# Performance work log

Hardware: AMD Instinct MI355X
Metric: run time of the kernel (lower is better)

Reference implementation:

```python
import jax, jax.numpy as jnp
import numpy as np

SEQ, B, DIM, UNITS = 256, 64, 1024, 1024


def setup_inputs() -> dict:
    key = jax.random.key(0)
    k1, k2, k3, k4, k5, k6 = jax.random.split(key, 6)
    s = 1.0 / np.sqrt(UNITS)
    x = jax.random.normal(k1, (SEQ, B, DIM), dtype=jnp.float32)
    hx = jnp.zeros((B, UNITS), dtype=jnp.float32)
    cx = jnp.zeros((B, UNITS), dtype=jnp.float32)
    reset = (jax.random.uniform(k2, (SEQ, B, 1)) < 0.05).astype(jnp.float32)
    W_ih = jax.random.uniform(k3, (4 * UNITS, DIM), minval=-s, maxval=s, dtype=jnp.float32)
    W_hh = jax.random.uniform(k4, (4 * UNITS, UNITS), minval=-s, maxval=s, dtype=jnp.float32)
    b_ih = jax.random.uniform(k5, (4 * UNITS,), minval=-s, maxval=s, dtype=jnp.float32)
    b_hh = jax.random.uniform(k6, (4 * UNITS,), minval=-s, maxval=s, dtype=jnp.float32)
    return {"x": x, "hx": hx, "cx": cx, "reset": reset,
            "W_ih": W_ih, "W_hh": W_hh, "b_ih": b_ih, "b_hh": b_hh}


def _lstm_scan(x, hx, cx, mask, W_ih, W_hh, b_ih, b_hh):
    # Precompute input projections for all timesteps in one big GEMM:
    # [seq, b, dim] @ [dim, 4u] -> [seq, b, 4u]
    x_proj = jnp.einsum('sbd,gd->sbg', x, W_ih) + b_ih + b_hh

    def step(carry, inp):
        h, c = carry
        xp_t, m_t = inp               # xp_t: [b, 4u], m_t: [b, 1]
        h = h * m_t                   # reset hidden/cell state at episode starts
        c = c * m_t
        gates = xp_t + h @ W_hh.T     # [b, 4u]
        i, f, g, o = jnp.split(gates, 4, axis=-1)  # torch LSTMCell gate order
        i = jax.nn.sigmoid(i)
        f = jax.nn.sigmoid(f)
        g = jnp.tanh(g)
        o = jax.nn.sigmoid(o)
        c = f * c + i * g
        h = o * jnp.tanh(c)
        return (h, c), (h, c)

    (_, _), (hs, cs) = jax.lax.scan(step, (hx, cx), (x_proj, mask))
    return hs, cs  # each [seq, b, units]


def reference(x, hx, cx, reset, W_ih, W_hh, b_ih, b_hh):
    mask = 1.0 - reset  # [seq, b, 1]
    hs, cs = _lstm_scan(x, hx, cx, mask, W_ih, W_hh, b_ih, b_hh)
    # original returns (stacked outputs, per-step (h, c) states)
    return hs, hs, cs
```

## Files before the change

### kernel.cpp

```cpp
#include <hip/hip_runtime.h>
#include <stdint.h>

typedef unsigned short ushort_t;
typedef __attribute__((ext_vector_type(8))) short s16x8;
typedef __attribute__((ext_vector_type(4))) float f32x4;
typedef __attribute__((ext_vector_type(4))) unsigned short u16x4;

#define TO_GLB(p) ((const __attribute__((address_space(1))) void*)(p))
#define TO_LDS(p) ((__attribute__((address_space(3))) void*)(p))

__device__ __forceinline__ ushort_t f2bf(float f) {
  union { float f; uint32_t u; } v; v.f = f;
  uint32_t u = v.u;
  uint32_t r = (u + 0x7FFFu + ((u >> 16) & 1u)) >> 16;
  return (ushort_t)r;
}
__device__ __forceinline__ float bf2f(ushort_t b) {
  union { uint32_t u; float f; } v; v.u = ((uint32_t)b) << 16;
  return v.f;
}
__device__ __forceinline__ float sigm(float x) {
  x = fminf(fmaxf(x, -30.f), 30.f);
  return 1.0f / (1.0f + __expf(-x));
}
__device__ __forceinline__ float tanh_f(float x) {
  x = fminf(fmaxf(x, -15.f), 15.f);
  float t = __expf(2.0f * x);
  return (t - 1.0f) / (t + 1.0f);
}

__global__ void conv_f32_to_bf16(const float* __restrict__ src,
                                 ushort_t* __restrict__ dst, int n4) {
  int i = blockIdx.x * blockDim.x + threadIdx.x;
  if (i < n4) {
    float4 v = ((const float4*)src)[i];
    u16x4 o;
    o[0] = f2bf(v.x); o[1] = f2bf(v.y); o[2] = f2bf(v.z); o[3] = f2bf(v.w);
    *(u16x4*)(dst + 4 * (size_t)i) = o;
  }
}

__global__ void init_h(const float* __restrict__ hx, ushort_t* __restrict__ h0, int n) {
  int i = blockIdx.x * blockDim.x + threadIdx.x;
  if (i < n) h0[i] = f2bf(hx[i]);
}

__global__ __launch_bounds__(256) void gemm_xproj(
    const ushort_t* __restrict__ A,
    const ushort_t* __restrict__ Bw,
    const float* __restrict__ b_ih, const float* __restrict__ b_hh,
    ushort_t* __restrict__ C)
{
  __shared__ ushort_t As[128 * 32];
  __shared__ ushort_t Bs[128 * 32];
  const int t = threadIdx.x;
  const int lane = t & 63;
  const int wid = t >> 6;
  const int wr = wid >> 1, wc = wid & 1;
  const size_t tm = (size_t)blockIdx.x * 128;
  const size_t tn = (size_t)blockIdx.y * 128;

  f32x4 acc[4][4];
  const f32x4 zero = {0.f, 0.f, 0.f, 0.f};
#pragma unroll
  for (int m = 0; m < 4; m++)
#pragma unroll
    for (int n = 0; n < 4; n++) acc[m][n] = zero;

  for (int k0 = 0; k0 < 1024; k0 += 32) {
    __syncthreads();
#pragma unroll
    for (int i = 0; i < 2; i++) {
      int row = i * 64 + (t >> 2);
      int kc = (t & 3) * 8;
      const ushort_t* ga = A + (tm + row) * 1024 + k0 + kc;
      __builtin_amdgcn_global_load_lds(TO_GLB(ga),
          TO_LDS((char*)As + (i * 256 + wid * 64) * 16), 16, 0, 0);
      const ushort_t* gb = Bw + (tn + row) * 1024 + k0 + kc;
      __builtin_amdgcn_global_load_lds(TO_GLB(gb),
          TO_LDS((char*)Bs + (i * 256 + wid * 64) * 16), 16, 0, 0);
    }
    __syncthreads();
    s16x8 af[4], bfr[4];
#pragma unroll
    for (int m = 0; m < 4; m++) {
      int r = wr * 64 + m * 16 + (lane & 15);
      af[m] = *(const s16x8*)((const char*)As + r * 64 + (lane >> 4) * 16);
    }
#pragma unroll
    for (int n = 0; n < 4; n++) {
      int r = wc * 64 + n * 16 + (lane & 15);
      bfr[n] = *(const s16x8*)((const char*)Bs + r * 64 + (lane >> 4) * 16);
    }
#pragma unroll
    for (int m = 0; m < 4; m++)
#pragma unroll
      for (int n = 0; n < 4; n++)
        acc[m][n] = __builtin_amdgcn_mfma_f32_16x16x32_bf16(af[m], bfr[n], acc[m][n], 0, 0, 0);
  }

#pragma unroll
  for (int m = 0; m < 4; m++)
#pragma unroll
    for (int n = 0; n < 4; n++)
#pragma unroll
      for (int j = 0; j < 4; j++) {
        size_t row = tm + wr * 64 + m * 16 + ((lane >> 4) << 2) + j;
        int col = (int)tn + wc * 64 + n * 16 + (lane & 15);
        float v = acc[m][n][j] + b_ih[col] + b_hh[col];
        C[row * 4096 + col] = f2bf(v);
      }
}

__global__ __launch_bounds__(512, 2) void lstm_scan(
    const ushort_t* __restrict__ whhb,
    const ushort_t* __restrict__ xproj,
    const float* __restrict__ reset,
    const float* __restrict__ cx,
    ushort_t* __restrict__ h0buf, ushort_t* __restrict__ h1buf,
    unsigned int* __restrict__ flags,
    float* __restrict__ out_h0, float* __restrict__ out_h1,
    float* __restrict__ out_cs)
{
  __shared__ char smem[40960];
  char* hs = smem;
  float* gsh = (float*)(smem + 32768);

  const int t = threadIdx.x;
  const int lane = t & 63;
  const int w = t >> 6;
  const int j16 = lane & 15;
  const int q = lane >> 4;
  const int blk = blockIdx.x;
  const int bg = blk >> 5;
  const int ug = blk & 31;
  const int b0 = bg * 16;
  const int u0 = ug * 32;

  s16x8 bfrag[32];
  {
    int lr = w * 16 + j16;
    int g = lr >> 5, lu = lr & 31;
    const ushort_t* wrow = whhb + ((size_t)(g * 1024 + u0 + lu)) * 1024 + q * 8;
#pragma unroll
    for (int kk = 0; kk < 32; kk++)
      bfrag[kk] = *(const s16x8*)(wrow + kk * 32);
  }
#pragma unroll
  for (int kk = 0; kk < 32; kk++)
    asm volatile("" : "+v"(bfrag[kk]));

  const int b_local = t >> 5;
  const int lu_t = t & 31;
  float c_reg = cx[(size_t)(b0 + b_local) * 1024 + u0 + lu_t];

  const int sr = t & 15;
  const int sc = t >> 4;

  for (int s = 0; s < 256; s++) {
    const ushort_t* hc = (s & 1) ? h1buf : h0buf;
    ushort_t* hn = (s & 1) ? h0buf : h1buf;

    const size_t xb = ((size_t)s * 64 + b0 + b_local) * 4096 + u0 + lu_t;
    ushort_t xp0 = xproj[xb];
    ushort_t xp1 = xproj[xb + 1024];
    ushort_t xp2 = xproj[xb + 2048];
    ushort_t xp3 = xproj[xb + 3072];
    float m2 = 1.0f - reset[s * 64 + b0 + b_local];
    float mrow = reset[s * 64 + b0 + sr];

    if (s > 0) {
      if (w == 0 && lane < 32) {
        const unsigned int* fp = flags + bg * 32 + lane;
        while (__hip_atomic_load(fp, __ATOMIC_RELAXED, __HIP_MEMORY_SCOPE_AGENT)
               < (unsigned int)s) {}
      }
      __syncthreads();
    }

    {
      const char* src = (const char*)(hc + (size_t)(b0 + sr) * 1024 + sc * 32);
#pragma unroll
      for (int jj = 0; jj < 8; jj++) {
        unsigned long long v = __hip_atomic_load(
            (const unsigned long long*)(src + jj * 8),
            __ATOMIC_RELAXED, __HIP_MEMORY_SCOPE_AGENT);
        if (mrow != 0.0f) v = 0ull;
        int off = (sr * 2048 + sc * 64 + jj * 8) ^ ((sr & 7) << 4);
        *(unsigned long long*)(hs + off) = v;
      }
    }
    __syncthreads();

    f32x4 acc0 = {0.f, 0.f, 0.f, 0.f}, acc1 = {0.f, 0.f, 0.f, 0.f};
#pragma unroll
    for (int kk = 0; kk < 32; kk += 2) {
      int off0 = (j16 * 2048 + kk * 64 + q * 16) ^ ((j16 & 7) << 4);
      int off1 = (j16 * 2048 + (kk + 1) * 64 + q * 16) ^ ((j16 & 7) << 4);
      s16x8 a0 = *(const s16x8*)(hs + off0);
      s16x8 a1 = *(const s16x8*)(hs + off1);
      acc0 = __builtin_amdgcn_mfma_f32_16x16x32_bf16(a0, bfrag[kk], acc0, 0, 0, 0);
      acc1 = __builtin_amdgcn_mfma_f32_16x16x32_bf16(a1, bfrag[kk + 1], acc1, 0, 0, 0);
    }

#pragma unroll
    for (int jj = 0; jj < 4; jj++) {
      int row = q * 4 + jj;
      int col = (w * 16 + j16) ^ ((row & 7) << 2);
      gsh[row * 128 + col] = acc0[jj] + acc1[jj];
    }
    __syncthreads();

    float gv0 = gsh[b_local * 128 + ((0 * 32 + lu_t) ^ ((b_local & 7) << 2))] + bf2f(xp0);
    float gv1 = gsh[b_local * 128 + ((1 * 32 + lu_t) ^ ((b_local & 7) << 2))] + bf2f(xp1);
    float gv2 = gsh[b_local * 128 + ((2 * 32 + lu_t) ^ ((b_local & 7) << 2))] + bf2f(xp2);
    float gv3 = gsh[b_local * 128 + ((3 * 32 + lu_t) ^ ((b_local & 7) << 2))] + bf2f(xp3);
    float ii = sigm(gv0), ff = sigm(gv1), G = tanh_f(gv2), oo = sigm(gv3);
    float cn = ff * (c_reg * m2) + ii * G;
    float hv = oo * tanh_f(cn);
    c_reg = cn;

    {
      unsigned int mybits = (unsigned int)f2bf(hv);
      unsigned int pb = (unsigned int)__shfl_xor((int)mybits, 1, 64);
      if ((t & 1) == 0) {
        unsigned int pack = mybits | (pb << 16);
        __hip_atomic_store(
            (unsigned int*)(hn + (size_t)(b0 + b_local) * 1024 + u0 + lu_t),
            pack, __ATOMIC_RELAXED, __HIP_MEMORY_SCOPE_AGENT);
      }
    }

    asm volatile("s_waitcnt vmcnt(0)" ::: "memory");
    __syncthreads();
    if (t == 0)
      __hip_atomic_store(&flags[blk], (unsigned int)(s + 1),
                         __ATOMIC_RELAXED, __HIP_MEMORY_SCOPE_AGENT);

    size_t ob = ((size_t)s * 64 + b0 + b_local) * 1024 + u0 + lu_t;
    out_cs[ob] = cn;
    out_h0[ob] = hv;
    out_h1[ob] = hv;
  }
}

extern "C" void kernel_launch(void* const* d_in, const int* in_sizes, int n_in,
                              void* d_out, int out_size, void* d_ws, size_t ws_size,
                              hipStream_t stream) {
  const float* x     = (const float*)d_in[0];
  const float* hx    = (const float*)d_in[1];
  const float* cx    = (const float*)d_in[2];
  const float* reset = (const float*)d_in[3];
  const float* W_ih  = (const float*)d_in[4];
  const float* W_hh  = (const float*)d_in[5];
  const float* b_ih  = (const float*)d_in[6];
  const float* b_hh  = (const float*)d_in[7];
  float* out = (float*)d_out;

  char* ws = (char*)d_ws;
  ushort_t* xbf   = (ushort_t*)(ws);
  ushort_t* wihb  = (ushort_t*)(ws + 33554432);
  ushort_t* whhb  = (ushort_t*)(ws + 41943040);
  ushort_t* xproj = (ushort_t*)(ws + 50331648);
  ushort_t* h0    = (ushort_t*)(ws + 184549376);
  ushort_t* h1    = (ushort_t*)(ws + 184680448);
  unsigned int* flags = (unsigned int*)(ws + 184811520);

  hipMemsetAsync(flags, 0, 128 * sizeof(unsigned int), stream);
  hipLaunchKernelGGL(conv_f32_to_bf16, dim3(16384), dim3(256), 0, stream, x, xbf, 4194304);
  hipLaunchKernelGGL(conv_f32_to_bf16, dim3(4096), dim3(256), 0, stream, W_ih, wihb, 1048576);
  hipLaunchKernelGGL(conv_f32_to_bf16, dim3(4096), dim3(256), 0, stream, W_hh, whhb, 1048576);
  hipLaunchKernelGGL(init_h, dim3(256), dim3(256), 0, stream, hx, h0, 65536);
  hipLaunchKernelGGL(gemm_xproj, dim3(128, 32), dim3(256), 0, stream, xbf, wihb, b_ih, b_hh, xproj);

  float* oh0 = out;
  float* oh1 = out + 16777216;
  float* ocs = out + 33554432;

  const ushort_t* whhb_c = whhb;
  const ushort_t* xproj_c = xproj;
  void* args[] = {(void*)&whhb_c, (void*)&xproj_c, (void*)&reset, (void*)&cx,
                  (void*)&h0, (void*)&h1, (void*)&flags,
                  (void*)&oh0, (void*)&oh1, (void*)&ocs};
  hipLaunchCooperativeKernel((void*)lstm_scan, dim3(128), dim3(512), args, 0, stream);
}
```

Before: 1.516 ms.

## Split recurrent scan across 256 blocks with K-split MFMA and per-wave flag polling

The persistent LSTM scan now runs on 256 blocks instead of 128, each handling 16 hidden units. Each block splits the K dimension across two wave halves and reduces the partial gate sums through shared memory, which halves the per-block recurrent work and register-resident weights. Every wave now polls the 64 producer flags itself, replacing a single polling wave plus a barrier. The h-state is loaded with wide cache-bypassing loads. In exchange, each step synchronises across more blocks, only half the threads do the elementwise update, and more flag polling traffic is generated.

```diff
diff --git a/kernel.cpp b/kernel.cpp
--- a/kernel.cpp
+++ b/kernel.cpp
@@ -122,111 +122,121 @@
     float* __restrict__ out_h0, float* __restrict__ out_h1,
     float* __restrict__ out_cs)
 {
-  __shared__ char smem[40960];
+  __shared__ char smem[43520];
   char* hs = smem;
   float* gsh = (float*)(smem + 32768);
 
   const int t = threadIdx.x;
   const int lane = t & 63;
   const int w = t >> 6;
+  const int ns = w & 3;
+  const int kh = w >> 2;
   const int j16 = lane & 15;
   const int q = lane >> 4;
   const int blk = blockIdx.x;
-  const int bg = blk >> 5;
-  const int ug = blk & 31;
+  const int bg = blk >> 6;
+  const int ug = blk & 63;
   const int b0 = bg * 16;
-  const int u0 = ug * 32;
-
-  s16x8 bfrag[32];
+  const int u0 = ug * 16;
+
+  s16x8 bfrag[16];
   {
-    int lr = w * 16 + j16;
-    int g = lr >> 5, lu = lr & 31;
-    const ushort_t* wrow = whhb + ((size_t)(g * 1024 + u0 + lu)) * 1024 + q * 8;
-#pragma unroll
-    for (int kk = 0; kk < 32; kk++)
+    const ushort_t* wrow = whhb + ((size_t)(ns * 1024 + u0 + j16)) * 1024 + kh * 512 + q * 8;
+#pragma unroll
+    for (int kk = 0; kk < 16; kk++)
       bfrag[kk] = *(const s16x8*)(wrow + kk * 32);
   }
 #pragma unroll
-  for (int kk = 0; kk < 32; kk++)
+  for (int kk = 0; kk < 16; kk++)
     asm volatile("" : "+v"(bfrag[kk]));
 
-  const int b_local = t >> 5;
-  const int lu_t = t & 31;
-  float c_reg = cx[(size_t)(b0 + b_local) * 1024 + u0 + lu_t];
+  const int b_local = t >> 4;
+  const int lu = t & 15;
+  const bool upd = (t < 256);
+  float c_reg = 0.0f;
+  if (upd) c_reg = cx[(size_t)(b0 + b_local) * 1024 + u0 + lu];
 
   const int sr = t & 15;
   const int sc = t >> 4;
+  const int swz = (sr & 7) << 4;
+  const s16x8 zv = {0, 0, 0, 0, 0, 0, 0, 0};
+  const f32x4 fzero = {0.f, 0.f, 0.f, 0.f};
 
   for (int s = 0; s < 256; s++) {
     const ushort_t* hc = (s & 1) ? h1buf : h0buf;
     ushort_t* hn = (s & 1) ? h0buf : h1buf;
 
-    const size_t xb = ((size_t)s * 64 + b0 + b_local) * 4096 + u0 + lu_t;
-    ushort_t xp0 = xproj[xb];
-    ushort_t xp1 = xproj[xb + 1024];
-    ushort_t xp2 = xproj[xb + 2048];
-    ushort_t xp3 = xproj[xb + 3072];
-    float m2 = 1.0f - reset[s * 64 + b0 + b_local];
+    float xv0 = 0.f, xv1 = 0.f, xv2 = 0.f, xv3 = 0.f, m2 = 0.f;
+    if (upd) {
+      const ushort_t* xpp = xproj + ((size_t)s * 64 + b0 + b_local) * 4096 + u0 + lu;
+      xv0 = bf2f(xpp[0]);
+      xv1 = bf2f(xpp[1024]);
+      xv2 = bf2f(xpp[2048]);
+      xv3 = bf2f(xpp[3072]);
+      m2 = 1.0f - reset[s * 64 + b0 + b_local];
+    }
     float mrow = reset[s * 64 + b0 + sr];
 
     if (s > 0) {
-      if (w == 0 && lane < 32) {
-        const unsigned int* fp = flags + bg * 32 + lane;
-        while (__hip_atomic_load(fp, __ATOMIC_RELAXED, __HIP_MEMORY_SCOPE_AGENT)
-               < (unsigned int)s) {}
-      }
-      __syncthreads();
+      const unsigned int* fp = flags + bg * 64 + lane;
+      while (__hip_atomic_load(fp, __ATOMIC_RELAXED, __HIP_MEMORY_SCOPE_AGENT)
+             < (unsigned int)s) {}
+      asm volatile("" ::: "memory");
     }
 
     {
-      const char* src = (const char*)(hc + (size_t)(b0 + sr) * 1024 + sc * 32);
-#pragma unroll
-      for (int jj = 0; jj < 8; jj++) {
-        unsigned long long v = __hip_atomic_load(
-            (const unsigned long long*)(src + jj * 8),
-            __ATOMIC_RELAXED, __HIP_MEMORY_SCOPE_AGENT);
-        if (mrow != 0.0f) v = 0ull;
-        int off = (sr * 2048 + sc * 64 + jj * 8) ^ ((sr & 7) << 4);
-        *(unsigned long long*)(hs + off) = v;
-      }
-    }
-    __syncthreads();
-
-    f32x4 acc0 = {0.f, 0.f, 0.f, 0.f}, acc1 = {0.f, 0.f, 0.f, 0.f};
-#pragma unroll
-    for (int kk = 0; kk < 32; kk += 2) {
-      int off0 = (j16 * 2048 + kk * 64 + q * 16) ^ ((j16 & 7) << 4);
-      int off1 = (j16 * 2048 + (kk + 1) * 64 + q * 16) ^ ((j16 & 7) << 4);
-      s16x8 a0 = *(const s16x8*)(hs + off0);
-      s16x8 a1 = *(const s16x8*)(hs + off1);
-      acc0 = __builtin_amdgcn_mfma_f32_16x16x32_bf16(a0, bfrag[kk], acc0, 0, 0, 0);
-      acc1 = __builtin_amdgcn_mfma_f32_16x16x32_bf16(a1, bfrag[kk + 1], acc1, 0, 0, 0);
-    }
-
-#pragma unroll
-    for (int jj = 0; jj < 4; jj++) {
-      int row = q * 4 + jj;
-      int col = (w * 16 + j16) ^ ((row & 7) << 2);
-      gsh[row * 128 + col] = acc0[jj] + acc1[jj];
-    }
-    __syncthreads();
-
-    float gv0 = gsh[b_local * 128 + ((0 * 32 + lu_t) ^ ((b_local & 7) << 2))] + bf2f(xp0);
-    float gv1 = gsh[b_local * 128 + ((1 * 32 + lu_t) ^ ((b_local & 7) << 2))] + bf2f(xp1);
-    float gv2 = gsh[b_local * 128 + ((2 * 32 + lu_t) ^ ((b_local & 7) << 2))] + bf2f(xp2);
-    float gv3 = gsh[b_local * 128 + ((3 * 32 + lu_t) ^ ((b_local & 7) << 2))] + bf2f(xp3);
-    float ii = sigm(gv0), ff = sigm(gv1), G = tanh_f(gv2), oo = sigm(gv3);
-    float cn = ff * (c_reg * m2) + ii * G;
-    float hv = oo * tanh_f(cn);
-    c_reg = cn;
-
-    {
+      const char* srcp = (const char*)(hc + (size_t)(b0 + sr) * 1024 + sc * 32);
+      s16x8 v0, v1, v2, v3;
+      asm volatile("global_load_dwordx4 %0, %1, off sc0 sc1" : "=v"(v0) : "v"(srcp));
+      asm volatile("global_load_dwordx4 %0, %1, off offset:16 sc0 sc1" : "=v"(v1) : "v"(srcp));
+      asm volatile("global_load_dwordx4 %0, %1, off offset:32 sc0 sc1" : "=v"(v2) : "v"(srcp));
+      asm volatile("global_load_dwordx4 %0, %1, off offset:48 sc0 sc1" : "=v"(v3) : "v"(srcp));
+      asm volatile("s_waitcnt vmcnt(0)" ::: "memory");
+      __builtin_amdgcn_sched_barrier(0);
+      if (mrow != 0.0f) { v0 = zv; v1 = zv; v2 = zv; v3 = zv; }
+      const int base = sr * 2048 + sc * 64;
+      *(s16x8*)(hs + ((base + 0)  ^ swz)) = v0;
+      *(s16x8*)(hs + ((base + 16) ^ swz)) = v1;
+      *(s16x8*)(hs + ((base + 32) ^ swz)) = v2;
+      *(s16x8*)(hs + ((base + 48) ^ swz)) = v3;
+    }
+    __syncthreads();
+
+    f32x4 acc = fzero;
+#pragma unroll
+    for (int kk = 0; kk < 16; kk++) {
+      int off = (j16 * 2048 + kh * 1024 + kk * 64 + q * 16) ^ ((j16 & 7) << 4);
+      s16x8 a = *(const s16x8*)(hs + off);
+      acc = __builtin_amdgcn_mfma_f32_16x16x32_bf16(a, bfrag[kk], acc, 0, 0, 0);
+    }
+#pragma unroll
+    for (int kk = 0; kk < 16; kk++)
+      asm volatile("" : "+v"(bfrag[kk]));
+
+#pragma unroll
+    for (int jj = 0; jj < 4; jj++)
+      gsh[kh * 1344 + (q * 4 + jj) * 84 + ns * 16 + j16] = acc[jj];
+    __syncthreads();
+
+    float hv = 0.0f, cn = 0.0f;
+    if (upd) {
+      const float* g0p = gsh + b_local * 84;
+      const float* g1p = gsh + 1344 + b_local * 84;
+      float gv0 = g0p[lu]      + g1p[lu]      + xv0;
+      float gv1 = g0p[16 + lu] + g1p[16 + lu] + xv1;
+      float gv2 = g0p[32 + lu] + g1p[32 + lu] + xv2;
+      float gv3 = g0p[48 + lu] + g1p[48 + lu] + xv3;
+      float ii = sigm(gv0), ff = sigm(gv1), G = tanh_f(gv2), oo = sigm(gv3);
+      cn = ff * (c_reg * m2) + ii * G;
+      hv = oo * tanh_f(cn);
+      c_reg = cn;
+
       unsigned int mybits = (unsigned int)f2bf(hv);
       unsigned int pb = (unsigned int)__shfl_xor((int)mybits, 1, 64);
       if ((t & 1) == 0) {
         unsigned int pack = mybits | (pb << 16);
         __hip_atomic_store(
-            (unsigned int*)(hn + (size_t)(b0 + b_local) * 1024 + u0 + lu_t),
+            (unsigned int*)(hn + (size_t)(b0 + b_local) * 1024 + u0 + lu),
             pack, __ATOMIC_RELAXED, __HIP_MEMORY_SCOPE_AGENT);
       }
     }
@@ -237,10 +247,12 @@
       __hip_atomic_store(&flags[blk], (unsigned int)(s + 1),
                          __ATOMIC_RELAXED, __HIP_MEMORY_SCOPE_AGENT);
 
-    size_t ob = ((size_t)s * 64 + b0 + b_local) * 1024 + u0 + lu_t;
-    out_cs[ob] = cn;
-    out_h0[ob] = hv;
-    out_h1[ob] = hv;
+    if (upd) {
+      size_t ob = ((size_t)s * 64 + b0 + b_local) * 1024 + u0 + lu;
+      out_cs[ob] = cn;
+      out_h0[ob] = hv;
+      out_h1[ob] = hv;
+    }
   }
 }
 
@@ -266,7 +278,7 @@
   ushort_t* h1    = (ushort_t*)(ws + 184680448);
   unsigned int* flags = (unsigned int*)(ws + 184811520);
 
-  hipMemsetAsync(flags, 0, 128 * sizeof(unsigned int), stream);
+  hipMemsetAsync(flags, 0, 256 * sizeof(unsigned int), stream);
   hipLaunchKernelGGL(conv_f32_to_bf16, dim3(16384), dim3(256), 0, stream, x, xbf, 4194304);
   hipLaunchKernelGGL(conv_f32_to_bf16, dim3(4096), dim3(256), 0, stream, W_ih, wihb, 1048576);
   hipLaunchKernelGGL(conv_f32_to_bf16, dim3(4096), dim3(256), 0, stream, W_hh, whhb, 1048576);
@@ -282,5 +294,5 @@
   void* args[] = {(void*)&whhb_c, (void*)&xproj_c, (void*)&reset, (void*)&cx,
                   (void*)&h0, (void*)&h1, (void*)&flags,
                   (void*)&oh0, (void*)&oh1, (void*)&ocs};
-  hipLaunchCooperativeKernel((void*)lstm_scan, dim3(128), dim3(512), args, 0, stream);
-}
+  hipLaunchCooperativeKernel((void*)lstm_scan, dim3(256), dim3(512), args, 0, stream);
+}
```

After: 1.518 ms. Within noise of the previous version (+0.1%).
